# Performance work log

Hardware: AMD Instinct MI355X
Metric: run time of the kernel (lower is better)

## Reference

```python
import jax, jax.numpy as jnp
import numpy as np

B, LQ, LKV = 2, 2048, 1024
DQ = DK = DV_IN = 512
H, DQK, DV = 8, 64, 64
DOUT = 512
SPAN, STRIDE = 128, 2


def setup_inputs() -> dict:
    key = jax.random.key(0)
    ks = jax.random.split(key, 7)
    W_SCALE = 0.05  # keep pre-softmax logits in a sane range
    return {
        "q": jax.random.normal(ks[0], (B, LQ, DQ), jnp.float32),
        "k": jax.random.normal(ks[1], (B, LKV, DK), jnp.float32),
        "v": jax.random.normal(ks[2], (B, LKV, DV_IN), jnp.float32),
        "Wq": jax.random.normal(ks[3], (DQ, H * DQK), jnp.float32) * W_SCALE,
        "Wk": jax.random.normal(ks[4], (DK, H * DQK), jnp.float32) * W_SCALE,
        "Wv": jax.random.normal(ks[5], (DV_IN, H * DV), jnp.float32) * W_SCALE,
        "Wout": jax.random.normal(ks[6], (H * DV, DOUT), jnp.float32) * W_SCALE,
        "head_num": H,
        "span": SPAN,
        "stride": STRIDE,
    }


def reference(q, k, v, Wq, Wk, Wv, Wout, head_num, span, stride):
    batch, length_q, _ = q.shape
    length_kv = k.shape[1]
    width = -(-span // stride)  # ceil(span / stride)
    hd_qk = Wq.shape[1] // head_num
    hd_v = Wv.shape[1] // head_num

    Q = (q @ Wq).reshape(batch, length_q, head_num, hd_qk)
    K = (k @ Wk).reshape(batch, length_kv, head_num, hd_qk)
    V = (v @ Wv).reshape(batch, length_kv, head_num, hd_v)

    # Local-window indices: query j attends kv position j//stride + w - (width-1)
    j = jnp.arange(length_q)[:, None]            # [Lq, 1]
    w = jnp.arange(width)[None, :]               # [1, width]
    orig_col = w - (width - 1) + j // stride     # [Lq, width]
    valid = (orig_col >= 0) & (orig_col < length_kv) & \
            ((j % stride) <= span - 1 - (width - w - 1) * stride)
    mask = jnp.where(valid, 0.0, -jnp.inf).astype(q.dtype)
    idx = jnp.clip(orig_col, 0, length_kv - 1)   # masked entries are dont-care

    Kg = K[:, idx]                               # [B, Lq, width, H, dQK]
    # NOTE: original module applies NO 1/sqrt(d) scaling
    scores = jnp.einsum('bjhd,bjwhd->bhjw', Q, Kg) + mask[None, None]
    p = jax.nn.softmax(scores, axis=-1)          # [B, H, Lq, width]

    Vg = V[:, idx]                               # [B, Lq, width, H, dV]
    out = jnp.einsum('bhjw,bjwhd->bjhd', p, Vg)
    out = out.reshape(batch, length_q, head_num * hd_v)
    return out @ Wout
```

## Files before the change

kernel.cpp:

```cpp
#include <hip/hip_runtime.h>
#include <stdint.h>

typedef _Float16 f16;
typedef _Float16 f16x8 __attribute__((ext_vector_type(8)));
typedef float f32x4 __attribute__((ext_vector_type(4)));

#define LQn   2048
#define LKVn  1024
#define DM    512
#define NH    8
#define WSZ   262144

static __device__ __forceinline__ f32x4 mfma_f16(f16x8 a, f16x8 b, f32x4 c) {
  return __builtin_amdgcn_mfma_f32_16x16x32_f16(a, b, c, 0, 0, 0);
}

__global__ __launch_bounds__(256) void transpose_w_kernel(
    const float* __restrict__ Wq, const float* __restrict__ Wk,
    const float* __restrict__ Wv, const float* __restrict__ Wo,
    f16* __restrict__ WTf) {
  __shared__ float tile[64 * 65];
  const int bid = blockIdx.x;
  const int mat = bid >> 6;
  const int tb  = bid & 63;
  const int r0 = (tb >> 3) * 64;
  const int c0 = (tb & 7) * 64;
  const float* W = (mat == 0) ? Wq : (mat == 1) ? Wk : (mat == 2) ? Wv : Wo;
  const int t = threadIdx.x;
#pragma unroll
  for (int i = 0; i < 16; ++i) {
    int idx = i * 256 + t;
    int r = idx >> 6, c = idx & 63;
    tile[r * 65 + c] = W[(size_t)(r0 + r) * DM + c0 + c];
  }
  __syncthreads();
#pragma unroll
  for (int i = 0; i < 16; ++i) {
    int idx = i * 256 + t;
    int r = idx >> 6, c = idx & 63;
    int n = c0 + r, kk = r0 + c;
    int n16 = n >> 4, ln = n & 15;
    int it = kk >> 5, h4 = (kk >> 3) & 3, e = kk & 7;
    int lane = h4 * 16 + ln;
    WTf[(size_t)mat * WSZ + ((size_t)(n16 * 16 + it) * 64 + lane) * 8 + e] =
        (f16)tile[c * 65 + r];
  }
}

__global__ __launch_bounds__(512) void proj_kernel(
    const float* __restrict__ q, const float* __restrict__ k,
    const float* __restrict__ v, const f16* __restrict__ WTf,
    f16* __restrict__ Qf, f16* __restrict__ Kf, f16* __restrict__ Vf) {
  __shared__ f16 smA[32 * 512];
  const int bid = blockIdx.x;
  const float* A;
  const f16* Bf;
  f16* C;
  int m0;
  if (bid < 128)      { A = q; Bf = WTf;            C = Qf; m0 = bid * 32; }
  else if (bid < 192) { A = k; Bf = WTf + WSZ;      C = Kf; m0 = (bid - 128) * 32; }
  else                { A = v; Bf = WTf + 2 * WSZ;  C = Vf; m0 = (bid - 192) * 32; }

  const int t = threadIdx.x;
  const int lane = t & 63;
  const int w = t >> 6;
  const int ln = lane & 15, hi4 = lane >> 4;

#pragma unroll
  for (int i = 0; i < 4; ++i) {
    int idx = i * 512 + t;
    int r = idx >> 6, u = idx & 63;
    const float* g = A + (size_t)(m0 + r) * 512 + u * 8;
    f32x4 x0 = *(const f32x4*)g, x1 = *(const f32x4*)(g + 4);
    f16x8 hv;
#pragma unroll
    for (int e = 0; e < 4; ++e) { hv[e] = (f16)x0[e]; hv[4 + e] = (f16)x1[e]; }
    int phys = (u & ~7) | ((u & 7) ^ (r & 7));
    *(f16x8*)&smA[r * 512 + phys * 8] = hv;
  }
  __syncthreads();

  const f16* gB = Bf + ((size_t)(w * 4) * 16 * 64 + lane) * 8;
  const f32x4 zf = {0.f, 0.f, 0.f, 0.f};
  f32x4 acc[2][4];
#pragma unroll
  for (int a = 0; a < 2; ++a)
#pragma unroll
    for (int b = 0; b < 4; ++b) acc[a][b] = zf;

  f16x8 buf0[4], buf1[4];
#pragma unroll
  for (int nf = 0; nf < 4; ++nf) buf0[nf] = *(const f16x8*)(gB + nf * 8192);
#pragma unroll
  for (int nf = 0; nf < 4; ++nf) buf1[nf] = *(const f16x8*)(gB + nf * 8192 + 512);

#pragma unroll
  for (int it = 0; it < 16; ++it) {
    f16x8 bfr[4], ah[2];
#pragma unroll
    for (int nf = 0; nf < 4; ++nf) bfr[nf] = (it & 1) ? buf1[nf] : buf0[nf];
    if (it + 2 < 16) {
#pragma unroll
      for (int nf = 0; nf < 4; ++nf) {
        f16x8 nv = *(const f16x8*)(gB + nf * 8192 + (it + 2) * 512);
        if (it & 1) buf1[nf] = nv; else buf0[nf] = nv;
      }
    }
#pragma unroll
    for (int mf = 0; mf < 2; ++mf) {
      int row = mf * 16 + ln;
      int uu = it * 4 + hi4;
      int phys = (uu & ~7) | ((uu & 7) ^ (row & 7));
      ah[mf] = *(const f16x8*)&smA[row * 512 + phys * 8];
    }
#pragma unroll
    for (int mf = 0; mf < 2; ++mf)
#pragma unroll
      for (int nf = 0; nf < 4; ++nf)
        acc[mf][nf] = mfma_f16(ah[mf], bfr[nf], acc[mf][nf]);
  }

#pragma unroll
  for (int mf = 0; mf < 2; ++mf)
#pragma unroll
    for (int nf = 0; nf < 4; ++nf)
#pragma unroll
      for (int e = 0; e < 4; ++e) {
        size_t off = (size_t)(m0 + mf * 16 + hi4 * 4 + e) * 512 +
                     w * 64 + nf * 16 + ln;
        C[off] = (f16)acc[mf][nf][e];
      }
}

__global__ __launch_bounds__(512) void outproj_kernel(
    const f16* __restrict__ AO, const f16* __restrict__ WTf,
    float* __restrict__ out) {
  __shared__ f16 smA[16 * 512];
  const int bid = blockIdx.x;
  const int m0 = bid * 16;
  const f16* Bf = WTf + (size_t)3 * WSZ;
  const int t = threadIdx.x;
  const int lane = t & 63;
  const int w = t >> 6;
  const int ln = lane & 15, hi4 = lane >> 4;

#pragma unroll
  for (int i = 0; i < 2; ++i) {
    int idx = i * 512 + t;
    int r = idx >> 6, u = idx & 63;
    f16x8 hv = *(const f16x8*)(AO + (size_t)(m0 + r) * 512 + u * 8);
    int phys = (u & ~7) | ((u & 7) ^ (r & 7));
    *(f16x8*)&smA[r * 512 + phys * 8] = hv;
  }
  __syncthreads();

  const f16* gB = Bf + ((size_t)(w * 4) * 16 * 64 + lane) * 8;
  const f32x4 zf = {0.f, 0.f, 0.f, 0.f};
  f32x4 acc[4];
#pragma unroll
  for (int b = 0; b < 4; ++b) acc[b] = zf;

  f16x8 buf0[4], buf1[4];
#pragma unroll
  for (int nf = 0; nf < 4; ++nf) buf0[nf] = *(const f16x8*)(gB + nf * 8192);
#pragma unroll
  for (int nf = 0; nf < 4; ++nf) buf1[nf] = *(const f16x8*)(gB + nf * 8192 + 512);

#pragma unroll
  for (int it = 0; it < 16; ++it) {
    f16x8 bfr[4], av;
#pragma unroll
    for (int nf = 0; nf < 4; ++nf) bfr[nf] = (it & 1) ? buf1[nf] : buf0[nf];
    if (it + 2 < 16) {
#pragma unroll
      for (int nf = 0; nf < 4; ++nf) {
        f16x8 nv = *(const f16x8*)(gB + nf * 8192 + (it + 2) * 512);
        if (it & 1) buf1[nf] = nv; else buf0[nf] = nv;
      }
    }
    {
      int uu = it * 4 + hi4;
      int phys = (uu & ~7) | ((uu & 7) ^ (ln & 7));
      av = *(const f16x8*)&smA[ln * 512 + phys * 8];
    }
#pragma unroll
    for (int nf = 0; nf < 4; ++nf)
      acc[nf] = mfma_f16(av, bfr[nf], acc[nf]);
  }

#pragma unroll
  for (int nf = 0; nf < 4; ++nf)
#pragma unroll
    for (int e = 0; e < 4; ++e)
      out[(size_t)(m0 + hi4 * 4 + e) * 512 + w * 64 + nf * 16 + ln] = acc[nf][e];
}

__global__ __launch_bounds__(512, 2) void attn_kernel(
    const f16* __restrict__ Qf, const f16* __restrict__ Kf,
    const f16* __restrict__ Vf, f16* __restrict__ AO) {
  __shared__ f16 smQ[128 * 64];
  __shared__ f16 smK[128 * 64];
  __shared__ f16 smVt[64 * 128];
  __shared__ f16 smP[128 * 128];
  const int bid = blockIdx.x;
  const int qt = bid & 15;
  const int h  = (bid >> 4) & 7;
  const int b  = bid >> 7;
  const int j0 = qt * 128;
  const int pbase = (j0 >> 1) - 63;
  const int t = threadIdx.x;
  const int lane = t & 63, w = t >> 6;
  const int ln = lane & 15, hi4 = lane >> 4;

#pragma unroll
  for (int i = 0; i < 2; ++i) {
    int idx = i * 512 + t;
    int r = idx >> 3, u = idx & 7;
    int sw = r * 64 + ((u ^ (r & 7)) * 8);
    size_t qoff = ((size_t)(b * LQn + j0 + r)) * 512 + h * 64 + u * 8;
    *(f16x8*)&smQ[sw] = *(const f16x8*)(Qf + qoff);
    int p = pbase + r;
    p = p < 0 ? 0 : (p > LKVn - 1 ? LKVn - 1 : p);
    size_t koff = ((size_t)(b * LKVn + p)) * 512 + h * 64 + u * 8;
    *(f16x8*)&smK[sw] = *(const f16x8*)(Kf + koff);
    f16x8 vv = *(const f16x8*)(Vf + koff);
#pragma unroll
    for (int e = 0; e < 8; ++e) {
      int rv = u * 8 + e;
      smVt[rv * 128 + (((r >> 3) ^ (rv & 15)) * 8) + (r & 7)] = vv[e];
    }
  }
  __syncthreads();

  const f32x4 zf = {0.f, 0.f, 0.f, 0.f};
  f32x4 s[8];
#pragma unroll
  for (int cf = 0; cf < 8; ++cf) s[cf] = zf;
#pragma unroll
  for (int kk = 0; kk < 64; kk += 32) {
    const int ub = kk >> 3;
    int addrq = (w * 16 + ln) * 64 + (((ub + hi4) ^ (ln & 7)) * 8);
    f16x8 ah = *(const f16x8*)&smQ[addrq];
#pragma unroll
    for (int cf = 0; cf < 8; ++cf) {
      int addrk = (cf * 16 + ln) * 64 + (((ub + hi4) ^ (ln & 7)) * 8);
      f16x8 bh = *(const f16x8*)&smK[addrk];
      s[cf] = mfma_f16(ah, bh, s[cf]);
    }
  }

#pragma unroll
  for (int r = 0; r < 4; ++r) {
    int rloc = w * 16 + hi4 * 4 + r;
    int wlo = rloc >> 1;
    int colmin = wlo > -pbase ? wlo : -pbase;
    int colmax = wlo + 63;
    float sv[8];
    float mx = -1e30f;
#pragma unroll
    for (int cf = 0; cf < 8; ++cf) {
      int col = cf * 16 + ln;
      float val = s[cf][r];
      bool ok = (col >= colmin) && (col <= colmax);
      sv[cf] = ok ? val : -1e30f;
      mx = fmaxf(mx, sv[cf]);
    }
#pragma unroll
    for (int msk = 1; msk < 16; msk <<= 1) mx = fmaxf(mx, __shfl_xor(mx, msk, 64));
    float sum = 0.f;
#pragma unroll
    for (int cf = 0; cf < 8; ++cf) {
      sv[cf] = __expf(sv[cf] - mx);
      sum += sv[cf];
    }
#pragma unroll
    for (int msk = 1; msk < 16; msk <<= 1) sum += __shfl_xor(sum, msk, 64);
    float rs = 1.0f / sum;
#pragma unroll
    for (int cf = 0; cf < 8; ++cf) {
      int uu = cf * 2 + (ln >> 3);
      smP[rloc * 128 + ((uu ^ (rloc & 15)) * 8) + (ln & 7)] = (f16)(sv[cf] * rs);
    }
  }
  __syncthreads();

  f32x4 o[4];
#pragma unroll
  for (int nf = 0; nf < 4; ++nf) o[nf] = zf;
#pragma unroll
  for (int kk = 0; kk < 128; kk += 32) {
    const int ub = kk >> 3;
    f16x8 pa = *(const f16x8*)&smP[(w * 16 + ln) * 128 + (((ub + hi4) ^ ln) * 8)];
#pragma unroll
    for (int nf = 0; nf < 4; ++nf) {
      int d = nf * 16 + ln;
      f16x8 vf = *(const f16x8*)&smVt[d * 128 + (((ub + hi4) ^ ln) * 8)];
      o[nf] = mfma_f16(pa, vf, o[nf]);
    }
  }

#pragma unroll
  for (int nf = 0; nf < 4; ++nf)
#pragma unroll
    for (int e = 0; e < 4; ++e) {
      int rloc = w * 16 + hi4 * 4 + e;
      AO[((size_t)(b * LQn + j0 + rloc)) * 512 + h * 64 + nf * 16 + ln] =
          (f16)o[nf][e];
    }
}

extern "C" void kernel_launch(void* const* d_in, const int* in_sizes, int n_in,
                              void* d_out, int out_size, void* d_ws, size_t ws_size,
                              hipStream_t stream) {
  const float* q    = (const float*)d_in[0];
  const float* k    = (const float*)d_in[1];
  const float* v    = (const float*)d_in[2];
  const float* Wq   = (const float*)d_in[3];
  const float* Wk   = (const float*)d_in[4];
  const float* Wv   = (const float*)d_in[5];
  const float* Wout = (const float*)d_in[6];
  float* out = (float*)d_out;

  char* ws = (char*)d_ws;
  f16* WTf = (f16*)ws;
  f16* Qf  = (f16*)(ws + (size_t)(2 << 20));
  f16* Kf  = (f16*)(ws + (size_t)(6 << 20));
  f16* Vf  = (f16*)(ws + (size_t)(8 << 20));
  f16* AO  = (f16*)(ws + (size_t)(10 << 20));

  transpose_w_kernel<<<256, 256, 0, stream>>>(Wq, Wk, Wv, Wout, WTf);
  proj_kernel<<<256, 512, 0, stream>>>(q, k, v, WTf, Qf, Kf, Vf);
  attn_kernel<<<256, 512, 0, stream>>>(Qf, Kf, Vf, AO);
  outproj_kernel<<<256, 512, 0, stream>>>(AO, WTf, out);
}
```

Measured before the change: 39.44 us.

## Shrink attention query tile to 64 rows with 96-key window; deepen weight prefetch

The attention kernel now handles 64 query rows per block instead of 128, so each tile needs only a 96-row K/V window. This removes the QK and PV MFMA work on key columns that were always masked, and doubles the block count to 512 of 256 threads. Separately, both projection GEMMs now prefetch four B-fragment stages ahead instead of two to hide global load latency, at the cost of more live registers. The smaller tiles also mean more redundant K/V reloads per query, since neighbouring blocks' windows overlap.

```diff
diff --git a/kernel.cpp b/kernel.cpp
--- a/kernel.cpp
+++ b/kernel.cpp
@@ -88,23 +88,23 @@
 #pragma unroll
     for (int b = 0; b < 4; ++b) acc[a][b] = zf;
 
-  f16x8 buf0[4], buf1[4];
-#pragma unroll
-  for (int nf = 0; nf < 4; ++nf) buf0[nf] = *(const f16x8*)(gB + nf * 8192);
-#pragma unroll
-  for (int nf = 0; nf < 4; ++nf) buf1[nf] = *(const f16x8*)(gB + nf * 8192 + 512);
+  f16x8 pb[4][4];
+#pragma unroll
+  for (int pp = 0; pp < 4; ++pp)
+#pragma unroll
+    for (int nf = 0; nf < 4; ++nf)
+      pb[pp][nf] = *(const f16x8*)(gB + nf * 8192 + pp * 512);
 
 #pragma unroll
   for (int it = 0; it < 16; ++it) {
+    const int slot = it & 3;
     f16x8 bfr[4], ah[2];
 #pragma unroll
-    for (int nf = 0; nf < 4; ++nf) bfr[nf] = (it & 1) ? buf1[nf] : buf0[nf];
-    if (it + 2 < 16) {
-#pragma unroll
-      for (int nf = 0; nf < 4; ++nf) {
-        f16x8 nv = *(const f16x8*)(gB + nf * 8192 + (it + 2) * 512);
-        if (it & 1) buf1[nf] = nv; else buf0[nf] = nv;
-      }
+    for (int nf = 0; nf < 4; ++nf) bfr[nf] = pb[slot][nf];
+    if (it + 4 < 16) {
+#pragma unroll
+      for (int nf = 0; nf < 4; ++nf)
+        pb[slot][nf] = *(const f16x8*)(gB + nf * 8192 + (it + 4) * 512);
     }
 #pragma unroll
     for (int mf = 0; mf < 2; ++mf) {
@@ -160,23 +160,23 @@
 #pragma unroll
   for (int b = 0; b < 4; ++b) acc[b] = zf;
 
-  f16x8 buf0[4], buf1[4];
-#pragma unroll
-  for (int nf = 0; nf < 4; ++nf) buf0[nf] = *(const f16x8*)(gB + nf * 8192);
-#pragma unroll
-  for (int nf = 0; nf < 4; ++nf) buf1[nf] = *(const f16x8*)(gB + nf * 8192 + 512);
+  f16x8 pb[4][4];
+#pragma unroll
+  for (int pp = 0; pp < 4; ++pp)
+#pragma unroll
+    for (int nf = 0; nf < 4; ++nf)
+      pb[pp][nf] = *(const f16x8*)(gB + nf * 8192 + pp * 512);
 
 #pragma unroll
   for (int it = 0; it < 16; ++it) {
+    const int slot = it & 3;
     f16x8 bfr[4], av;
 #pragma unroll
-    for (int nf = 0; nf < 4; ++nf) bfr[nf] = (it & 1) ? buf1[nf] : buf0[nf];
-    if (it + 2 < 16) {
-#pragma unroll
-      for (int nf = 0; nf < 4; ++nf) {
-        f16x8 nv = *(const f16x8*)(gB + nf * 8192 + (it + 2) * 512);
-        if (it & 1) buf1[nf] = nv; else buf0[nf] = nv;
-      }
+    for (int nf = 0; nf < 4; ++nf) bfr[nf] = pb[slot][nf];
+    if (it + 4 < 16) {
+#pragma unroll
+      for (int nf = 0; nf < 4; ++nf)
+        pb[slot][nf] = *(const f16x8*)(gB + nf * 8192 + (it + 4) * 512);
     }
     {
       int uu = it * 4 + hi4;
@@ -195,18 +195,18 @@
       out[(size_t)(m0 + hi4 * 4 + e) * 512 + w * 64 + nf * 16 + ln] = acc[nf][e];
 }
 
-__global__ __launch_bounds__(512, 2) void attn_kernel(
+__global__ __launch_bounds__(256, 2) void attn_kernel(
     const f16* __restrict__ Qf, const f16* __restrict__ Kf,
     const f16* __restrict__ Vf, f16* __restrict__ AO) {
-  __shared__ f16 smQ[128 * 64];
-  __shared__ f16 smK[128 * 64];
+  __shared__ f16 smQ[64 * 64];
+  __shared__ f16 smK[96 * 64];
   __shared__ f16 smVt[64 * 128];
-  __shared__ f16 smP[128 * 128];
+  __shared__ f16 smP[64 * 128];
   const int bid = blockIdx.x;
-  const int qt = bid & 15;
-  const int h  = (bid >> 4) & 7;
-  const int b  = bid >> 7;
-  const int j0 = qt * 128;
+  const int qt = bid & 31;
+  const int h  = (bid >> 5) & 7;
+  const int b  = bid >> 8;
+  const int j0 = qt * 64;
   const int pbase = (j0 >> 1) - 63;
   const int t = threadIdx.x;
   const int lane = t & 63, w = t >> 6;
@@ -214,11 +214,17 @@
 
 #pragma unroll
   for (int i = 0; i < 2; ++i) {
-    int idx = i * 512 + t;
+    int idx = i * 256 + t;
     int r = idx >> 3, u = idx & 7;
     int sw = r * 64 + ((u ^ (r & 7)) * 8);
     size_t qoff = ((size_t)(b * LQn + j0 + r)) * 512 + h * 64 + u * 8;
     *(f16x8*)&smQ[sw] = *(const f16x8*)(Qf + qoff);
+  }
+#pragma unroll
+  for (int i = 0; i < 3; ++i) {
+    int idx = i * 256 + t;
+    int r = idx >> 3, u = idx & 7;
+    int sw = r * 64 + ((u ^ (r & 7)) * 8);
     int p = pbase + r;
     p = p < 0 ? 0 : (p > LKVn - 1 ? LKVn - 1 : p);
     size_t koff = ((size_t)(b * LKVn + p)) * 512 + h * 64 + u * 8;
@@ -233,16 +239,16 @@
   __syncthreads();
 
   const f32x4 zf = {0.f, 0.f, 0.f, 0.f};
-  f32x4 s[8];
-#pragma unroll
-  for (int cf = 0; cf < 8; ++cf) s[cf] = zf;
+  f32x4 s[6];
+#pragma unroll
+  for (int cf = 0; cf < 6; ++cf) s[cf] = zf;
 #pragma unroll
   for (int kk = 0; kk < 64; kk += 32) {
     const int ub = kk >> 3;
     int addrq = (w * 16 + ln) * 64 + (((ub + hi4) ^ (ln & 7)) * 8);
     f16x8 ah = *(const f16x8*)&smQ[addrq];
 #pragma unroll
-    for (int cf = 0; cf < 8; ++cf) {
+    for (int cf = 0; cf < 6; ++cf) {
       int addrk = (cf * 16 + ln) * 64 + (((ub + hi4) ^ (ln & 7)) * 8);
       f16x8 bh = *(const f16x8*)&smK[addrk];
       s[cf] = mfma_f16(ah, bh, s[cf]);
@@ -255,10 +261,10 @@
     int wlo = rloc >> 1;
     int colmin = wlo > -pbase ? wlo : -pbase;
     int colmax = wlo + 63;
-    float sv[8];
+    float sv[6];
     float mx = -1e30f;
 #pragma unroll
-    for (int cf = 0; cf < 8; ++cf) {
+    for (int cf = 0; cf < 6; ++cf) {
       int col = cf * 16 + ln;
       float val = s[cf][r];
       bool ok = (col >= colmin) && (col <= colmax);
@@ -269,7 +275,7 @@
     for (int msk = 1; msk < 16; msk <<= 1) mx = fmaxf(mx, __shfl_xor(mx, msk, 64));
     float sum = 0.f;
 #pragma unroll
-    for (int cf = 0; cf < 8; ++cf) {
+    for (int cf = 0; cf < 6; ++cf) {
       sv[cf] = __expf(sv[cf] - mx);
       sum += sv[cf];
     }
@@ -277,7 +283,7 @@
     for (int msk = 1; msk < 16; msk <<= 1) sum += __shfl_xor(sum, msk, 64);
     float rs = 1.0f / sum;
 #pragma unroll
-    for (int cf = 0; cf < 8; ++cf) {
+    for (int cf = 0; cf < 6; ++cf) {
       int uu = cf * 2 + (ln >> 3);
       smP[rloc * 128 + ((uu ^ (rloc & 15)) * 8) + (ln & 7)] = (f16)(sv[cf] * rs);
     }
@@ -288,7 +294,7 @@
 #pragma unroll
   for (int nf = 0; nf < 4; ++nf) o[nf] = zf;
 #pragma unroll
-  for (int kk = 0; kk < 128; kk += 32) {
+  for (int kk = 0; kk < 96; kk += 32) {
     const int ub = kk >> 3;
     f16x8 pa = *(const f16x8*)&smP[(w * 16 + ln) * 128 + (((ub + hi4) ^ ln) * 8)];
 #pragma unroll
@@ -330,6 +336,6 @@
 
   transpose_w_kernel<<<256, 256, 0, stream>>>(Wq, Wk, Wv, Wout, WTf);
   proj_kernel<<<256, 512, 0, stream>>>(q, k, v, WTf, Qf, Kf, Vf);
-  attn_kernel<<<256, 512, 0, stream>>>(Qf, Kf, Vf, AO);
+  attn_kernel<<<512, 256, 0, stream>>>(Qf, Kf, Vf, AO);
   outproj_kernel<<<256, 512, 0, stream>>>(AO, WTf, out);
 }
```

After: 39.50 us. Within noise of the previous version (+0.2%).
